# Kernel tuning notes

Hardware: AMD Instinct MI355X
Metric: run time of the kernel (lower is better)

The kernel has to match this reference:

```python
import jax, jax.numpy as jnp
import numpy as np

N_SRC, N_MID, N_DST = 200000, 50000, 10000
D = 128
E1, E2 = 800000, 160000
EPS = 1e-12  # F.normalize eps


def setup_inputs() -> dict:
    key = jax.random.key(0)
    ks = jax.random.split(key, 12)
    s = 1.0 / np.sqrt(D)
    return {
        "x": jax.random.normal(ks[0], (N_SRC, D), jnp.float32),
        "W_l1": jax.random.uniform(ks[1], (D, D), jnp.float32, -s, s),
        "b_l1": jax.random.uniform(ks[2], (D,), jnp.float32, -s, s),
        "W_r1": jax.random.uniform(ks[3], (D, D), jnp.float32, -s, s),
        "W_l2": jax.random.uniform(ks[4], (D, D), jnp.float32, -s, s),
        "b_l2": jax.random.uniform(ks[5], (D,), jnp.float32, -s, s),
        "W_r2": jax.random.uniform(ks[6], (D, D), jnp.float32, -s, s),
        "row1": jax.random.randint(ks[7], (E1,), 0, N_SRC, jnp.int32),
        "col1": jax.random.randint(ks[8], (E1,), 0, N_MID, jnp.int32),
        "row2": jax.random.randint(ks[9], (E2,), 0, N_MID, jnp.int32),
        "col2": jax.random.randint(ks[10], (E2,), 0, N_DST, jnp.int32),
    }


def _sage_conv(x_src, x_dst, row, col, W_l, b_l, W_r, n_dst):
    # mean aggregation of source features over incoming edges (gather + scatter-add)
    msg = x_src[row]                                              # [E, D]
    agg = jax.ops.segment_sum(msg, col, num_segments=n_dst)       # [n_dst, D]
    deg = jax.ops.segment_sum(jnp.ones((row.shape[0],), x_src.dtype), col,
                              num_segments=n_dst)[:, None]        # [n_dst, 1]
    mean = jnp.where(deg > 0, agg / jnp.maximum(deg, 1.0), 0.0)
    out = mean @ W_l.T + b_l + x_dst @ W_r.T                      # lin_l + lin_r (root)
    # L2 normalize (normalize=True)
    norm = jnp.sqrt(jnp.sum(out * out, axis=-1, keepdims=True))
    return out / jnp.maximum(norm, EPS)


def reference(x, W_l1, b_l1, W_r1, W_l2, b_l2, W_r2, row1, col1, row2, col2):
    # layer 1: src = all sampled nodes, dst = first N_MID nodes
    h = _sage_conv(x, x[:N_MID], row1, col1, W_l1, b_l1, W_r1, N_MID)
    h = jax.nn.relu(h)  # dropout is identity in eval mode
    # layer 2: src = mid nodes, dst = first N_DST nodes (the batch targets)
    out = _sage_conv(h, h[:N_DST], row2, col2, W_l2, b_l2, W_r2, N_DST)
    return out
```

## Files before the change

kernel.cpp:

```cpp
#include <hip/hip_runtime.h>
#include <hip/hip_bf16.h>

#define DD 128
#define N_SRC 200000
#define N_MID 50000
#define N_DST 10000
#define E1 800000
#define E2 160000
#define CAP 48

#define BK_W  200
#define NB1   250
#define NB2   50
#define CCAP  3584
#define P1E   2048
#define NP1_1 ((E1 + P1E - 1) / P1E)
#define NP1_2 ((E2 + P1E - 1) / P1E)
#define P1_BLOCKS (NP1_1 + NP1_2)

typedef unsigned short u16;
typedef unsigned int u32;
typedef __attribute__((ext_vector_type(8))) short s16x8;
typedef __attribute__((ext_vector_type(4))) float f32x4;
typedef __attribute__((ext_vector_type(4))) float fv4;


__device__ __forceinline__ float bf_lo(u32 u) {
    union { u32 u; float f; } v; v.u = u << 16; return v.f;
}
__device__ __forceinline__ float bf_hi(u32 u) {
    union { u32 u; float f; } v; v.u = u & 0xffff0000u; return v.f;
}
__device__ __forceinline__ u32 f2bf_bits(float f) {
    union { float f; u32 u; } v; v.f = f;
    return (v.u + 0x7fffu + ((v.u >> 16) & 1u)) >> 16;
}
__device__ __forceinline__ u32 pack2bf(float lo, float hi) {
    return f2bf_bits(lo) | (f2bf_bits(hi) << 16);
}


#define NCONV8 (N_SRC * DD / 8)
#define WTF_T 8192
#define PREP_T (NCONV8 + WTF_T)
#define PREP_BLOCKS ((PREP_T + 255) / 256)
#define PA_BLOCKS (P1_BLOCKS + PREP_BLOCKS)

__global__ __launch_bounds__(256, 8) void prep_part(
    const float* __restrict__ x, u16* __restrict__ xb,
    const float* __restrict__ Wl1, const float* __restrict__ Wr1,
    u16* __restrict__ WTf1,
    const float* __restrict__ Wl2, const float* __restrict__ Wr2,
    u16* __restrict__ WTf2,
    const int* __restrict__ row1, const int* __restrict__ col1,
    const int* __restrict__ row2, const int* __restrict__ col2,
    int* __restrict__ ccnt1, int* __restrict__ ccnt2,
    int2* __restrict__ cbuf1, int2* __restrict__ cbuf2)
{
    __shared__ int lcnt[256];
    __shared__ int gbase[256];
    const int b = blockIdx.x;
    const int tid = threadIdx.x;

    if (b < P1_BLOCKS) {
        const int* __restrict__ colp;
        const int* __restrict__ rowp;
        int* __restrict__ ccnt;
        int2* __restrict__ cbuf;
        int e0, ne, nb;
        if (b < NP1_1) {
            colp = col1; rowp = row1; ccnt = ccnt1; cbuf = cbuf1;
            e0 = b * P1E; ne = E1 - e0; if (ne > P1E) ne = P1E; nb = NB1;
        } else {
            int bb = b - NP1_1;
            colp = col2; rowp = row2; ccnt = ccnt2; cbuf = cbuf2;
            e0 = bb * P1E; ne = E2 - e0; if (ne > P1E) ne = P1E; nb = NB2;
        }
        for (int t = tid; t < nb; t += 256) lcnt[t] = 0;
        __syncthreads();
        int ep[8];
        #pragma unroll
        for (int j = 0; j < 8; ++j) {
            int e = tid + j * 256;
            ep[j] = -1;
            if (e < ne) {
                int c = colp[e0 + e];
                int bk = c / BK_W;
                int rk = atomicAdd(&lcnt[bk], 1);
                ep[j] = (bk << 16) | rk;
            }
        }
        __syncthreads();
        for (int t = tid; t < nb; t += 256) {
            int c = lcnt[t];
            gbase[t] = c ? atomicAdd(&ccnt[t], c) : 0;
        }
        __syncthreads();
        #pragma unroll
        for (int j = 0; j < 8; ++j) {
            if (ep[j] >= 0) {
                int e = e0 + tid + j * 256;
                int bk = ep[j] >> 16;
                int pos = gbase[bk] + (ep[j] & 0xffff);
                if (pos < CCAP)
                    cbuf[(size_t)bk * CCAP + pos] = make_int2(colp[e], rowp[e]);
            }
        }
    } else {
        int i = (b - P1_BLOCKS) * 256 + tid;
        if (i < NCONV8) {
            const fv4* x4 = (const fv4*)x;
            fv4 a = __builtin_nontemporal_load(x4 + i * 2);
            fv4 bb = __builtin_nontemporal_load(x4 + i * 2 + 1);
            uint4 o;
            o.x = pack2bf(a[0], a[1]); o.y = pack2bf(a[2], a[3]);
            o.z = pack2bf(bb[0], bb[1]); o.w = pack2bf(bb[2], bb[3]);
            ((uint4*)xb)[i] = o;
        } else if (i < NCONV8 + WTF_T) {
            int t = i - NCONV8;
            int layer = t >> 12;
            int rem = t & 4095;
            int kt = rem >> 9;
            int nt = (rem >> 6) & 7;
            int lane = rem & 63;
            int gn = nt * 16 + (lane & 15);
            int k0 = kt * 32 + (lane >> 4) * 8;
            const float* Wl = layer ? Wl2 : Wl1;
            const float* Wr = layer ? Wr2 : Wr1;
            u16* WTf = layer ? WTf2 : WTf1;
            u32 o[4];
            #pragma unroll
            for (int p = 0; p < 4; ++p) {
                int ka = k0 + 2 * p, kb = ka + 1;
                float ea = (ka < 128) ? Wl[gn * 128 + ka] : Wr[gn * 128 + (ka - 128)];
                float eb = (kb < 128) ? Wl[gn * 128 + kb] : Wr[gn * 128 + (kb - 128)];
                o[p] = pack2bf(ea, eb);
            }
            ((uint4*)WTf)[(kt * 8 + nt) * 64 + lane] = make_uint4(o[0], o[1], o[2], o[3]);
        }
    }
}


__global__ __launch_bounds__(256, 8) void bucket_sort(
    const int2* __restrict__ cbuf1, const int2* __restrict__ cbuf2,
    const int* __restrict__ ccnt1, const int* __restrict__ ccnt2,
    int* __restrict__ cnt1, int* __restrict__ cnt2,
    int* __restrict__ csr1, int* __restrict__ csr2)
{
    const int b = blockIdx.x;
    const int tid = threadIdx.x;
    const int2* __restrict__ cbuf;
    const int* __restrict__ ccnt;
    int* __restrict__ cnt;
    int* __restrict__ csr;
    int bkt;
    if (b < NB1) { cbuf = cbuf1; ccnt = ccnt1; cnt = cnt1; csr = csr1; bkt = b; }
    else         { cbuf = cbuf2; ccnt = ccnt2; cnt = cnt2; csr = csr2; bkt = b - NB1; }
    const int col0 = bkt * BK_W;

    __shared__ int hist[BK_W];
    for (int t = tid; t < BK_W; t += 256) hist[t] = 0;
    __syncthreads();

    int n = ccnt[bkt]; if (n > CCAP) n = CCAP;
    const int2* bp = cbuf + (size_t)bkt * CCAP;
    for (int e = tid; e < n; e += 512) {
        int2 cr0 = bp[e];
        int e1i = e + 256;
        bool h1 = e1i < n;
        int2 cr1 = h1 ? bp[e1i] : cr0;
        int r0 = atomicAdd(&hist[cr0.x - col0], 1);
        if (r0 < CAP) csr[cr0.x * CAP + r0] = cr0.y;
        if (h1) {
            int r1 = atomicAdd(&hist[cr1.x - col0], 1);
            if (r1 < CAP) csr[cr1.x * CAP + r1] = cr1.y;
        }
    }
    __syncthreads();
    for (int t = tid; t < BK_W; t += 256) cnt[col0 + t] = hist[t];
}


template <int ROWS, bool RELU, int MINB>
__global__ __launch_bounds__(256, MINB) void sage_kernel(
    const u16* __restrict__ xsrc_b, const u16* __restrict__ xdst_b,
    const int* __restrict__ cnt, const int* __restrict__ csrf,
    const u16* __restrict__ WTf, const float* __restrict__ bias,
    float* __restrict__ out_f, u16* __restrict__ out_b,
    int n_dst, int fp32lim)
{
    __shared__ float smem[ROWS * 132];
    const int tid = threadIdx.x;
    const int i0 = blockIdx.x * ROWS;
    const int lane = tid & 63;
    const int w = tid >> 6;
    const int quarter = lane >> 4;
    const int l16 = lane & 15;
    const int half = lane >> 5;
    const int l32 = lane & 31;
    constexpr int RPW = ROWS / 4;

    const uint4* __restrict__ xs4 = (const uint4*)xsrc_b;
    const uint2* __restrict__ xd2 = (const uint2*)xdst_b;
    uint4* sA4 = (uint4*)smem;
    uint2* sA2 = (uint2*)smem;

    int degv = 0;
    {
        int rr = i0 + w * RPW + lane;
        if (lane < RPW && rr < n_dst) degv = cnt[rr];
    }
    int iv_next = 0;
    {
        int i = i0 + w * RPW;
        if (i < n_dst) iv_next = csrf[(size_t)i * CAP + lane];
    }

    for (int q = 0; q < RPW; ++q) {
        int r = w * RPW + q;
        int i = i0 + r;
        int deg = __shfl(degv, q);
        if (deg > CAP) deg = CAP;
        int iv = iv_next;
        if (q + 1 < RPW) {
            int i2 = i + 1;
            iv_next = (i2 < n_dst) ? csrf[(size_t)i2 * CAP + lane] : 0;
        }
        if (i < n_dst) {
            float acc[8] = {0.f, 0.f, 0.f, 0.f, 0.f, 0.f, 0.f, 0.f};
            if (deg > 0) {
                for (int g = 0; g < deg; g += 16) {
                    #pragma unroll
                    for (int j = 0; j < 4; ++j) {
                        if (g + 4 * j < deg) {
                            int rel = g + 4 * j + quarter;
                            int idx = __shfl(iv, rel & 63);
                            float m = (rel < deg) ? 1.f : 0.f;
                            uint4 u = xs4[(size_t)idx * 16 + l16];
                            acc[0] += m * bf_lo(u.x); acc[1] += m * bf_hi(u.x);
                            acc[2] += m * bf_lo(u.y); acc[3] += m * bf_hi(u.y);
                            acc[4] += m * bf_lo(u.z); acc[5] += m * bf_hi(u.z);
                            acc[6] += m * bf_lo(u.w); acc[7] += m * bf_hi(u.w);
                        }
                    }
                }
                #pragma unroll
                for (int k = 0; k < 8; ++k) {
                    acc[k] += __shfl_xor(acc[k], 16);
                    acc[k] += __shfl_xor(acc[k], 32);
                }
            }
            float s = (deg > 0) ? 1.f / (float)deg : 0.f;
            if (quarter == 0) {
                uint4 o;
                o.x = pack2bf(acc[0] * s, acc[1] * s);
                o.y = pack2bf(acc[2] * s, acc[3] * s);
                o.z = pack2bf(acc[4] * s, acc[5] * s);
                o.w = pack2bf(acc[6] * s, acc[7] * s);
                sA4[r * 33 + l16] = o;
            }
            if (half == 1) {
                sA2[r * 66 + 32 + l32] = xd2[(size_t)i * 32 + l32];
            }
        } else {
            if (quarter == 0) sA4[r * 33 + l16] = make_uint4(0, 0, 0, 0);
            if (half == 1)    sA2[r * 66 + 32 + l32] = make_uint2(0, 0);
        }
    }
    __syncthreads();

    constexpr int MT = ROWS / 16;
    const int nt0 = w * 2;
    const s16x8* sAv = (const s16x8*)smem;
    const s16x8* Bv = (const s16x8*)WTf;

    f32x4 C[MT][2];
    #pragma unroll
    for (int mt = 0; mt < MT; ++mt)
        #pragma unroll
        for (int ni = 0; ni < 2; ++ni)
            C[mt][ni] = (f32x4){0.f, 0.f, 0.f, 0.f};

    #pragma unroll
    for (int kt = 0; kt < 8; ++kt) {
        s16x8 a[MT];
        #pragma unroll
        for (int mt = 0; mt < MT; ++mt)
            a[mt] = sAv[(mt * 16 + l16) * 33 + kt * 4 + quarter];
        s16x8 b0 = Bv[(kt * 8 + nt0) * 64 + lane];
        s16x8 b1 = Bv[(kt * 8 + nt0 + 1) * 64 + lane];
        #pragma unroll
        for (int mt = 0; mt < MT; ++mt) {
            C[mt][0] = __builtin_amdgcn_mfma_f32_16x16x32_bf16(a[mt], b0, C[mt][0], 0, 0, 0);
            C[mt][1] = __builtin_amdgcn_mfma_f32_16x16x32_bf16(a[mt], b1, C[mt][1], 0, 0, 0);
        }
    }

    __syncthreads();
    float* sOut = smem;

    #pragma unroll
    for (int ni = 0; ni < 2; ++ni) {
        int col = (nt0 + ni) * 16 + l16;
        float bc = bias[col];
        #pragma unroll
        for (int mt = 0; mt < MT; ++mt) {
            #pragma unroll
            for (int r = 0; r < 4; ++r) {
                int row = mt * 16 + quarter * 4 + r;
                sOut[row * 132 + col] = C[mt][ni][r] + bc;
            }
        }
    }
    __syncthreads();

    constexpr int R = ROWS / 8;
    const int ty = tid >> 5;
    const int tx = tid & 31;
    #pragma unroll
    for (int r = 0; r < R; ++r) {
        int row = ty * R + r;
        float4 v = *(const float4*)(&sOut[row * 132 + tx * 4]);
        float s = v.x * v.x + v.y * v.y + v.z * v.z + v.w * v.w;
        #pragma unroll
        for (int off = 1; off < 32; off <<= 1) s += __shfl_xor(s, off);
        float scale = 1.f / fmaxf(sqrtf(s), 1e-12f);
        float v0 = v.x * scale, v1 = v.y * scale, v2 = v.z * scale, v3 = v.w * scale;
        if (RELU) {
            v0 = fmaxf(v0, 0.f); v1 = fmaxf(v1, 0.f);
            v2 = fmaxf(v2, 0.f); v3 = fmaxf(v3, 0.f);
        }
        int i = i0 + row;
        if (i < n_dst) {
            if (i < fp32lim)
                *(float4*)(out_f + (size_t)i * DD + tx * 4) = make_float4(v0, v1, v2, v3);
            if (out_b) {
                uint2 ob;
                ob.x = pack2bf(v0, v1);
                ob.y = pack2bf(v2, v3);
                *(uint2*)(out_b + (size_t)i * DD + tx * 4) = ob;
            }
        }
    }
}


extern "C" void kernel_launch(void* const* d_in, const int* in_sizes, int n_in,
                              void* d_out, int out_size, void* d_ws, size_t ws_size,
                              hipStream_t stream) {
    const float* x    = (const float*)d_in[0];
    const float* Wl1  = (const float*)d_in[1];
    const float* bl1  = (const float*)d_in[2];
    const float* Wr1  = (const float*)d_in[3];
    const float* Wl2  = (const float*)d_in[4];
    const float* bl2  = (const float*)d_in[5];
    const float* Wr2  = (const float*)d_in[6];
    const int* row1   = (const int*)d_in[7];
    const int* col1   = (const int*)d_in[8];
    const int* row2   = (const int*)d_in[9];
    const int* col2   = (const int*)d_in[10];
    float* out = (float*)d_out;

    char* p = (char*)d_ws;
    u16* xb    = (u16*)p;   p += (size_t)N_SRC * DD * sizeof(u16);
    char* hbv  = p;         p += (size_t)N_MID * DD * sizeof(u16);
    u16* hb    = (u16*)hbv;
    int2* cbuf1 = (int2*)hbv;
    int2* cbuf2 = cbuf1 + (size_t)NB1 * CCAP;
    u16* WTf1  = (u16*)p;   p += (size_t)256 * 128 * sizeof(u16);
    u16* WTf2  = (u16*)p;   p += (size_t)256 * 128 * sizeof(u16);
    char* zbase = p;
    int* ccnt1 = (int*)p;   p += 256 * sizeof(int);
    int* ccnt2 = (int*)p;   p += 64 * sizeof(int);
    int* cnt1  = (int*)p;   p += (size_t)N_MID * sizeof(int);
    int* cnt2  = (int*)p;   p += (size_t)N_DST * sizeof(int);
    int* csr1  = (int*)p;   p += (size_t)N_MID * CAP * sizeof(int);
    int* csr2  = (int*)p;   p += (size_t)N_DST * CAP * sizeof(int);
    p += 256;
    size_t zlen = (size_t)(p - zbase);

    (void)hipMemsetAsync(zbase, 0, zlen, stream);

    prep_part<<<PA_BLOCKS, 256, 0, stream>>>(
        x, xb, Wl1, Wr1, WTf1, Wl2, Wr2, WTf2,
        row1, col1, row2, col2, ccnt1, ccnt2, cbuf1, cbuf2);

    bucket_sort<<<NB1 + NB2, 256, 0, stream>>>(
        cbuf1, cbuf2, ccnt1, ccnt2, cnt1, cnt2, csr1, csr2);

    sage_kernel<32, true, 6><<<(N_MID + 31) / 32, 256, 0, stream>>>(
        xb, xb, cnt1, csr1, WTf1, bl1, (float*)nullptr, hb, N_MID, 0);

    sage_kernel<16, false, 6><<<(N_DST + 15) / 16, 256, 0, stream>>>(
        hb, hb, cnt2, csr2, WTf2, bl2, out, (u16*)nullptr, N_DST, N_DST);
}
```

Measured before the change: 252.4 us.

## Fuse bucket sort into layer-1 sage kernel with per-bucket flag handoff

Removes the separate bucket_sort launch. The first NROLE blocks of the layer-1 sage kernel claim and sort buckets through atomic CAS flags, and compute blocks spin-wait on, or sort themselves, the buckets covering their rows. The aggregation loop now gathers two destination rows together to expose more memory-level parallelism, and adds index clamping. In exchange it relies on inter-block spin-waiting, lowers the launch-bounds occupancy hint from 6 to 5, and moves cbuf out of the aliased hb buffer into its own workspace region.

Measured after the change: 693.4 us. 175% more time.

```diff
diff --git a/kernel.cpp b/kernel.cpp
--- a/kernel.cpp
+++ b/kernel.cpp
@@ -17,6 +17,7 @@
 #define NP1_1 ((E1 + P1E - 1) / P1E)
 #define NP1_2 ((E2 + P1E - 1) / P1E)
 #define P1_BLOCKS (NP1_1 + NP1_2)
+#define NROLE (NB1 + NB2)
 
 typedef unsigned short u16;
 typedef unsigned int u32;
@@ -142,34 +143,21 @@
 }
 
 
-__global__ __launch_bounds__(256, 8) void bucket_sort(
-    const int2* __restrict__ cbuf1, const int2* __restrict__ cbuf2,
-    const int* __restrict__ ccnt1, const int* __restrict__ ccnt2,
-    int* __restrict__ cnt1, int* __restrict__ cnt2,
-    int* __restrict__ csr1, int* __restrict__ csr2)
+__device__ __forceinline__ void sort_bucket(int bkt, const int2* __restrict__ cbuf,
+                                            const int* __restrict__ ccnt,
+                                            int* __restrict__ cnt, int* __restrict__ csr,
+                                            int* hist, int tid)
 {
-    const int b = blockIdx.x;
-    const int tid = threadIdx.x;
-    const int2* __restrict__ cbuf;
-    const int* __restrict__ ccnt;
-    int* __restrict__ cnt;
-    int* __restrict__ csr;
-    int bkt;
-    if (b < NB1) { cbuf = cbuf1; ccnt = ccnt1; cnt = cnt1; csr = csr1; bkt = b; }
-    else         { cbuf = cbuf2; ccnt = ccnt2; cnt = cnt2; csr = csr2; bkt = b - NB1; }
     const int col0 = bkt * BK_W;
-
-    __shared__ int hist[BK_W];
     for (int t = tid; t < BK_W; t += 256) hist[t] = 0;
     __syncthreads();
-
     int n = ccnt[bkt]; if (n > CCAP) n = CCAP;
     const int2* bp = cbuf + (size_t)bkt * CCAP;
     for (int e = tid; e < n; e += 512) {
         int2 cr0 = bp[e];
-        int e1i = e + 256;
-        bool h1 = e1i < n;
-        int2 cr1 = h1 ? bp[e1i] : cr0;
+        int e2 = e + 256;
+        bool h1 = e2 < n;
+        int2 cr1 = h1 ? bp[e2] : cr0;
         int r0 = atomicAdd(&hist[cr0.x - col0], 1);
         if (r0 < CAP) csr[cr0.x * CAP + r0] = cr0.y;
         if (h1) {
@@ -181,18 +169,68 @@
     for (int t = tid; t < BK_W; t += 256) cnt[col0 + t] = hist[t];
 }
 
+__device__ __forceinline__ void ensure_sorted(int bkt, const int2* __restrict__ cbuf,
+                                              const int* __restrict__ ccnt,
+                                              int* __restrict__ cnt, int* __restrict__ csr,
+                                              int* __restrict__ flags,
+                                              int* hist, int* stsh, int tid, bool wait)
+{
+    if (tid == 0) *stsh = atomicCAS(&flags[bkt], 0, 1);
+    __syncthreads();
+    int st = *stsh;
+    if (st == 0) {
+        sort_bucket(bkt, cbuf, ccnt, cnt, csr, hist, tid);
+        __threadfence();
+        __syncthreads();
+        if (tid == 0) atomicExch(&flags[bkt], 2);
+    } else if (st == 1 && wait) {
+        if (tid == 0) {
+            while (atomicAdd(&flags[bkt], 0) != 2) __builtin_amdgcn_s_sleep(16);
+        }
+        __syncthreads();
+    }
+    __threadfence();
+    __syncthreads();
+}
+
 
 template <int ROWS, bool RELU, int MINB>
 __global__ __launch_bounds__(256, MINB) void sage_kernel(
     const u16* __restrict__ xsrc_b, const u16* __restrict__ xdst_b,
-    const int* __restrict__ cnt, const int* __restrict__ csrf,
+    int* __restrict__ cnt, int* __restrict__ csrf,
     const u16* __restrict__ WTf, const float* __restrict__ bias,
     float* __restrict__ out_f, u16* __restrict__ out_b,
-    int n_dst, int fp32lim)
+    int n_dst, int fp32lim, int nsrc,
+    const int2* __restrict__ cbufA, const int* __restrict__ ccntA,
+    int* __restrict__ flagsA, int nbA,
+    const int2* __restrict__ cbufB, const int* __restrict__ ccntB,
+    int* __restrict__ cntB, int* __restrict__ csrB, int* __restrict__ flagsB,
+    int nrole)
 {
     __shared__ float smem[ROWS * 132];
+    __shared__ int hist[BK_W];
+    __shared__ int stsh;
     const int tid = threadIdx.x;
-    const int i0 = blockIdx.x * ROWS;
+
+    if (blockIdx.x < (u32)nrole) {
+        int rb = blockIdx.x;
+        if (rb < nbA)
+            ensure_sorted(rb, cbufA, ccntA, cnt, csrf, flagsA, hist, &stsh, tid, false);
+        else
+            ensure_sorted(rb - nbA, cbufB, ccntB, cntB, csrB, flagsB, hist, &stsh, tid, false);
+        return;
+    }
+
+    const int i0 = (blockIdx.x - nrole) * ROWS;
+
+    {
+        int b0 = i0 / BK_W;
+        int bl = (i0 + ROWS - 1) / BK_W; if (bl > nbA - 1) bl = nbA - 1;
+        ensure_sorted(b0, cbufA, ccntA, cnt, csrf, flagsA, hist, &stsh, tid, true);
+        if (bl != b0)
+            ensure_sorted(bl, cbufA, ccntA, cnt, csrf, flagsA, hist, &stsh, tid, true);
+    }
+
     const int lane = tid & 63;
     const int w = tid >> 6;
     const int quarter = lane >> 4;
@@ -211,61 +249,76 @@
         int rr = i0 + w * RPW + lane;
         if (lane < RPW && rr < n_dst) degv = cnt[rr];
     }
-    int iv_next = 0;
+    int ivA = 0, ivB = 0;
     {
-        int i = i0 + w * RPW;
-        if (i < n_dst) iv_next = csrf[(size_t)i * CAP + lane];
-    }
-
-    for (int q = 0; q < RPW; ++q) {
-        int r = w * RPW + q;
-        int i = i0 + r;
-        int deg = __shfl(degv, q);
-        if (deg > CAP) deg = CAP;
-        int iv = iv_next;
-        if (q + 1 < RPW) {
-            int i2 = i + 1;
-            iv_next = (i2 < n_dst) ? csrf[(size_t)i2 * CAP + lane] : 0;
-        }
-        if (i < n_dst) {
-            float acc[8] = {0.f, 0.f, 0.f, 0.f, 0.f, 0.f, 0.f, 0.f};
-            if (deg > 0) {
-                for (int g = 0; g < deg; g += 16) {
-                    #pragma unroll
-                    for (int j = 0; j < 4; ++j) {
-                        if (g + 4 * j < deg) {
-                            int rel = g + 4 * j + quarter;
-                            int idx = __shfl(iv, rel & 63);
-                            float m = (rel < deg) ? 1.f : 0.f;
-                            uint4 u = xs4[(size_t)idx * 16 + l16];
-                            acc[0] += m * bf_lo(u.x); acc[1] += m * bf_hi(u.x);
-                            acc[2] += m * bf_lo(u.y); acc[3] += m * bf_hi(u.y);
-                            acc[4] += m * bf_lo(u.z); acc[5] += m * bf_hi(u.z);
-                            acc[6] += m * bf_lo(u.w); acc[7] += m * bf_hi(u.w);
-                        }
-                    }
+        int iA = i0 + w * RPW;
+        if (iA < n_dst)     ivA = csrf[(size_t)iA * CAP + lane];
+        if (iA + 1 < n_dst) ivB = csrf[(size_t)(iA + 1) * CAP + lane];
+    }
+
+    for (int qq = 0; qq < RPW; qq += 2) {
+        int rA = w * RPW + qq, rB = rA + 1;
+        int iA = i0 + rA, iB = i0 + rB;
+        int degA = __shfl(degv, qq);     if (degA > CAP) degA = CAP;
+        int degB = __shfl(degv, qq + 1); if (degB > CAP) degB = CAP;
+        int curA = ivA, curB = ivB;
+        if (qq + 2 < RPW) {
+            int i2 = iA + 2, i3 = iA + 3;
+            ivA = (i2 < n_dst) ? csrf[(size_t)i2 * CAP + lane] : 0;
+            ivB = (i3 < n_dst) ? csrf[(size_t)i3 * CAP + lane] : 0;
+        }
+        float accA[8] = {0.f,0.f,0.f,0.f,0.f,0.f,0.f,0.f};
+        float accB[8] = {0.f,0.f,0.f,0.f,0.f,0.f,0.f,0.f};
+        int dmax = degA > degB ? degA : degB;
+        for (int g = 0; g < dmax; g += 16) {
+            #pragma unroll
+            for (int j = 0; j < 4; ++j) {
+                int rel = g + 4 * j + quarter;
+                if (g + 4 * j < degA) {
+                    int idx = __shfl(curA, rel & 63);
+                    idx = ((u32)idx < (u32)nsrc) ? idx : 0;
+                    float m = (rel < degA) ? 1.f : 0.f;
+                    uint4 u = xs4[(size_t)idx * 16 + l16];
+                    accA[0] += m * bf_lo(u.x); accA[1] += m * bf_hi(u.x);
+                    accA[2] += m * bf_lo(u.y); accA[3] += m * bf_hi(u.y);
+                    accA[4] += m * bf_lo(u.z); accA[5] += m * bf_hi(u.z);
+                    accA[6] += m * bf_lo(u.w); accA[7] += m * bf_hi(u.w);
                 }
-                #pragma unroll
-                for (int k = 0; k < 8; ++k) {
-                    acc[k] += __shfl_xor(acc[k], 16);
-                    acc[k] += __shfl_xor(acc[k], 32);
+                if (g + 4 * j < degB) {
+                    int idx = __shfl(curB, rel & 63);
+                    idx = ((u32)idx < (u32)nsrc) ? idx : 0;
+                    float m = (rel < degB) ? 1.f : 0.f;
+                    uint4 u = xs4[(size_t)idx * 16 + l16];
+                    accB[0] += m * bf_lo(u.x); accB[1] += m * bf_hi(u.x);
+                    accB[2] += m * bf_lo(u.y); accB[3] += m * bf_hi(u.y);
+                    accB[4] += m * bf_lo(u.z); accB[5] += m * bf_hi(u.z);
+                    accB[6] += m * bf_lo(u.w); accB[7] += m * bf_hi(u.w);
                 }
             }
-            float s = (deg > 0) ? 1.f / (float)deg : 0.f;
-            if (quarter == 0) {
-                uint4 o;
-                o.x = pack2bf(acc[0] * s, acc[1] * s);
-                o.y = pack2bf(acc[2] * s, acc[3] * s);
-                o.z = pack2bf(acc[4] * s, acc[5] * s);
-                o.w = pack2bf(acc[6] * s, acc[7] * s);
-                sA4[r * 33 + l16] = o;
-            }
-            if (half == 1) {
-                sA2[r * 66 + 32 + l32] = xd2[(size_t)i * 32 + l32];
-            }
-        } else {
-            if (quarter == 0) sA4[r * 33 + l16] = make_uint4(0, 0, 0, 0);
-            if (half == 1)    sA2[r * 66 + 32 + l32] = make_uint2(0, 0);
+        }
+        #pragma unroll
+        for (int k = 0; k < 8; ++k) {
+            accA[k] += __shfl_xor(accA[k], 16);
+            accA[k] += __shfl_xor(accA[k], 32);
+            accB[k] += __shfl_xor(accB[k], 16);
+            accB[k] += __shfl_xor(accB[k], 32);
+        }
+        float sA = (degA > 0) ? 1.f / (float)degA : 0.f;
+        float sB = (degB > 0) ? 1.f / (float)degB : 0.f;
+        if (quarter == 0) {
+            uint4 oA, oB;
+            oA.x = pack2bf(accA[0]*sA, accA[1]*sA); oA.y = pack2bf(accA[2]*sA, accA[3]*sA);
+            oA.z = pack2bf(accA[4]*sA, accA[5]*sA); oA.w = pack2bf(accA[6]*sA, accA[7]*sA);
+            oB.x = pack2bf(accB[0]*sB, accB[1]*sB); oB.y = pack2bf(accB[2]*sB, accB[3]*sB);
+            oB.z = pack2bf(accB[4]*sB, accB[5]*sB); oB.w = pack2bf(accB[6]*sB, accB[7]*sB);
+            sA4[rA * 33 + l16] = oA;
+            sA4[rB * 33 + l16] = oB;
+        }
+        if (half == 1) {
+            uint2 rootA = (iA < n_dst) ? xd2[(size_t)iA * 32 + l32] : make_uint2(0, 0);
+            uint2 rootB = (iB < n_dst) ? xd2[(size_t)iB * 32 + l32] : make_uint2(0, 0);
+            sA2[rA * 66 + 32 + l32] = rootA;
+            sA2[rB * 66 + 32 + l32] = rootB;
         }
     }
     __syncthreads();
@@ -364,21 +417,22 @@
 
     char* p = (char*)d_ws;
     u16* xb    = (u16*)p;   p += (size_t)N_SRC * DD * sizeof(u16);
-    char* hbv  = p;         p += (size_t)N_MID * DD * sizeof(u16);
-    u16* hb    = (u16*)hbv;
-    int2* cbuf1 = (int2*)hbv;
-    int2* cbuf2 = cbuf1 + (size_t)NB1 * CCAP;
+    u16* hb    = (u16*)p;   p += (size_t)N_MID * DD * sizeof(u16);
     u16* WTf1  = (u16*)p;   p += (size_t)256 * 128 * sizeof(u16);
     u16* WTf2  = (u16*)p;   p += (size_t)256 * 128 * sizeof(u16);
+    int2* cbuf1 = (int2*)p; p += (size_t)NB1 * CCAP * sizeof(int2);
+    int2* cbuf2 = (int2*)p; p += (size_t)NB2 * CCAP * sizeof(int2);
     char* zbase = p;
-    int* ccnt1 = (int*)p;   p += 256 * sizeof(int);
-    int* ccnt2 = (int*)p;   p += 64 * sizeof(int);
+    int* ccnt1  = (int*)p;  p += 256 * sizeof(int);
+    int* ccnt2  = (int*)p;  p += 64 * sizeof(int);
+    int* flags1 = (int*)p;  p += 256 * sizeof(int);
+    int* flags2 = (int*)p;  p += 64 * sizeof(int);
+    size_t zlen = (size_t)(p - zbase);
     int* cnt1  = (int*)p;   p += (size_t)N_MID * sizeof(int);
     int* cnt2  = (int*)p;   p += (size_t)N_DST * sizeof(int);
     int* csr1  = (int*)p;   p += (size_t)N_MID * CAP * sizeof(int);
     int* csr2  = (int*)p;   p += (size_t)N_DST * CAP * sizeof(int);
     p += 256;
-    size_t zlen = (size_t)(p - zbase);
 
     (void)hipMemsetAsync(zbase, 0, zlen, stream);
 
@@ -386,12 +440,13 @@
         x, xb, Wl1, Wr1, WTf1, Wl2, Wr2, WTf2,
         row1, col1, row2, col2, ccnt1, ccnt2, cbuf1, cbuf2);
 
-    bucket_sort<<<NB1 + NB2, 256, 0, stream>>>(
-        cbuf1, cbuf2, ccnt1, ccnt2, cnt1, cnt2, csr1, csr2);
-
-    sage_kernel<32, true, 6><<<(N_MID + 31) / 32, 256, 0, stream>>>(
-        xb, xb, cnt1, csr1, WTf1, bl1, (float*)nullptr, hb, N_MID, 0);
-
-    sage_kernel<16, false, 6><<<(N_DST + 15) / 16, 256, 0, stream>>>(
-        hb, hb, cnt2, csr2, WTf2, bl2, out, (u16*)nullptr, N_DST, N_DST);
-}
+    sage_kernel<32, true, 5><<<NROLE + (N_MID + 31) / 32, 256, 0, stream>>>(
+        xb, xb, cnt1, csr1, WTf1, bl1, (float*)nullptr, hb, N_MID, 0, N_SRC,
+        cbuf1, ccnt1, flags1, NB1,
+        cbuf2, ccnt2, cnt2, csr2, flags2, NROLE);
+
+    sage_kernel<16, false, 5><<<(N_DST + 15) / 16, 256, 0, stream>>>(
+        hb, hb, cnt2, csr2, WTf2, bl2, out, (u16*)nullptr, N_DST, N_DST, N_MID,
+        cbuf2, ccnt2, flags2, NB2,
+        cbuf2, ccnt2, cnt2, csr2, flags2, 0);
+}
```
